# Optimization experiments

Measured on AMD Instinct MI355X. Metric: run time of the kernel, lower is better.

Reference implementation:

```python
import jax, jax.numpy as jnp
import numpy as np

BS, TS, NA, OS = 32, 256, 16, 512
HID, D, W = 1024, 128, 8            # sw_hidden_dim, sw_input_dim, sw_window_size
OUT, DEC, NACT = 512, 512, 30       # sw_output_dim, sw_decoder_hidden_layer, n_actions


def setup_inputs() -> dict:
    key = jax.random.key(0)
    ks = jax.random.split(key, 12)
    p = lambda k, shape: jax.random.normal(k, shape, jnp.float32) * 0.02
    return {
        "inputs": jax.random.normal(ks[0], (BS, TS, NA, OS), jnp.float32),
        "hidden_state": jnp.zeros((BS, NA, (W - 1) * D), jnp.float32),
        "w1": p(ks[1], (OS, HID)),        "b1": jnp.zeros((HID,), jnp.float32),
        "w2": p(ks[2], (HID, D)),         "b2": jnp.zeros((D,), jnp.float32),
        "w3": p(ks[3], (W * D, OUT)),     "b3": jnp.zeros((OUT,), jnp.float32),
        "w4": p(ks[4], (OUT, DEC)),       "b4": jnp.zeros((DEC,), jnp.float32),
        "w5": p(ks[5], (DEC, NACT)),      "b5": jnp.zeros((NACT,), jnp.float32),
    }


def reference(inputs, hidden_state, w1, b1, w2, b2, w3, b3, w4, b4, w5, b5):
    bs, ts, na, _ = inputs.shape
    # encoder: two pointwise MLP layers over (bs, ts, na, *)
    x = jax.nn.relu(inputs @ w1 + b1)          # (bs, ts, na, HID)
    x = jax.nn.relu(x @ w2 + b2)               # (bs, ts, na, D)
    # build the full frame sequence: W-1 hidden frames followed by ts encoded frames
    hid_frames = hidden_state.reshape(bs, na, W - 1, D)
    seq = jnp.concatenate([hid_frames, jnp.transpose(x, (0, 2, 1, 3))], axis=2)  # (bs, na, ts+W-1, D)
    # sliding windows: window at step t = frames [t, t+W) — vectorized over all t
    wins = jnp.stack([seq[:, :, i:i + ts, :] for i in range(W)], axis=3)  # (bs, na, ts, W, D)
    wins = wins.reshape(bs, na, ts, W * D)
    h = jax.nn.relu(wins @ w3 + b3)            # (bs, na, ts, OUT)
    h = jnp.transpose(h, (0, 2, 1, 3))         # (bs, ts, na, OUT)
    h = jax.nn.relu(h @ w4 + b4)               # (bs, ts, na, DEC)
    q = h @ w5 + b5                            # (bs, ts, na, NACT)
    # final carried window: last W-1 frames of the sequence, flattened per agent
    window = seq[:, :, ts:, :].reshape(bs, na, (W - 1) * D)
    return (q, window)
```

## Files before the change

### kernel.cpp

```cpp
#include <hip/hip_runtime.h>
#include <hip/hip_bf16.h>
#include <hip/hip_fp8.h>


#define DEVI __device__ __forceinline__

typedef float f32x4 __attribute__((ext_vector_type(4)));
typedef short s16x8 __attribute__((ext_vector_type(8)));
typedef short s16x4 __attribute__((ext_vector_type(4)));
typedef long long i64;

#define ROWS 131072
#define SEQ_T 263

#define W2P_OFF 524288
#define W3P_OFF 655360
#define W4P_OFF 1179648
#define W5P_OFF 1441792
#define WP_TOTAL 1458176

#define W3P8_BYTE_OFF 2916352
#define SEQ8_BYTE_OFF 3440640
#define BIG_BYTE_OFF 37388288

DEVI short f2bf(float f) {
  union { __hip_bfloat16 h; short s; } u;
  u.h = __float2bfloat16(f);
  return u.s;
}

DEVI unsigned int f2e4(float f) {
  union { __hip_fp8_e4m3 h; unsigned char c; } u;
  u.h = __hip_fp8_e4m3(f);
  return (unsigned int)u.c;
}

#if __has_builtin(__builtin_amdgcn_cvt_pk_fp8_f32)
DEVI unsigned int pk4e4(float a, float b, float c, float d) {
  int v = 0;
  v = __builtin_amdgcn_cvt_pk_fp8_f32(a, b, v, false);
  v = __builtin_amdgcn_cvt_pk_fp8_f32(c, d, v, true);
  return (unsigned int)v;
}
#else
DEVI unsigned int pk4e4(float a, float b, float c, float d) {
  return f2e4(a) | (f2e4(b) << 8) | (f2e4(c) << 16) | (f2e4(d) << 24);
}
#endif

DEVI f32x4 MFMA(s16x8 a, s16x8 b, f32x4 c) {
  return __builtin_amdgcn_mfma_f32_16x16x32_bf16(a, b, c, 0, 0, 0);
}
DEVI f32x4 MFMA8(i64 a, i64 b, f32x4 c) {
  return __builtin_amdgcn_mfma_f32_16x16x32_fp8_fp8(a, b, c, 0, 0, 0);
}

__global__ __launch_bounds__(256) void pack_w_kernel(
    const float* __restrict__ w1, const float* __restrict__ w2,
    const float* __restrict__ w3, const float* __restrict__ w4,
    const float* __restrict__ w5, short* __restrict__ wp)
{
  int idx = blockIdx.x * 256 + threadIdx.x;
  const float* src; int sh, Nsrc, local;
  if (idx < W2P_OFF)      { src = w1; sh = 4; Nsrc = 1024; local = idx; }
  else if (idx < W3P_OFF) { src = w2; sh = 5; Nsrc = 128;  local = idx - W2P_OFF; }
  else if (idx < W4P_OFF) { src = w3; sh = 5; Nsrc = 512;  local = idx - W3P_OFF; }
  else if (idx < W5P_OFF) { src = w4; sh = 4; Nsrc = 512;  local = idx - W4P_OFF; }
  else                    { src = w5; sh = 4; Nsrc = 30;   local = idx - W5P_OFF; }
  int j    = local & 7;
  int lane = (local >> 3) & 63;
  int rest = local >> 9;
  int k0   = rest & ((1 << sh) - 1);
  int n0   = rest >> sh;
  int k = (k0 << 5) + ((lane >> 4) << 3) + j;
  int n = (n0 << 4) + (lane & 15);
  float v = (n < Nsrc) ? src[k * Nsrc + n] : 0.f;
  wp[idx] = f2bf(v);
}

__global__ __launch_bounds__(256) void pack_w_fp8_kernel(
    const float* __restrict__ w1, const float* __restrict__ w2,
    const float* __restrict__ w3,
    unsigned char* __restrict__ wp8, unsigned char* __restrict__ w3p8)
{
  int t = blockIdx.x * 256 + threadIdx.x;
  const float* src; int nkshift, Nsrc, dt; unsigned char* dst;
  if (t < 65536)      { src = w1; dt = t;         nkshift = 4; Nsrc = 1024; dst = wp8; }
  else if (t < 81920) { src = w2; dt = t - 65536; nkshift = 5; Nsrc = 128;  dst = wp8 + 524288; }
  else                { src = w3; dt = t - 81920; nkshift = 5; Nsrc = 512;  dst = w3p8; }
  int lane = dt & 63;
  int rest = dt >> 6;
  int k0   = rest & ((1 << nkshift) - 1);
  int n0   = rest >> nkshift;
  int kb = (k0 << 5) + ((lane >> 4) << 3);
  int n  = (n0 << 4) + (lane & 15);
  float v[8];
  #pragma unroll
  for (int j = 0; j < 8; ++j) v[j] = src[(kb + j) * Nsrc + n];
  unsigned long long pk = (unsigned long long)pk4e4(v[0], v[1], v[2], v[3])
                        | ((unsigned long long)pk4e4(v[4], v[5], v[6], v[7]) << 32);
  *(unsigned long long*)(dst + (long)dt * 8) = pk;
}

__global__ __launch_bounds__(256) void hid_copy_kernel(
    const float* __restrict__ hid, unsigned char* __restrict__ seq8)
{
  int t = blockIdx.x * 256 + threadIdx.x;
  int j = t & 15;
  int r = t >> 4;
  int i = r % 7;
  int ba = r / 7;
  int s = j ^ i;
  const float* src = hid + (r << 7) + (j << 3);
  f32x4 a = *(const f32x4*)src;
  f32x4 b = *(const f32x4*)(src + 4);
  unsigned long long pk = (unsigned long long)pk4e4(a[0], a[1], a[2], a[3])
                        | ((unsigned long long)pk4e4(b[0], b[1], b[2], b[3]) << 32);
  *(unsigned long long*)(seq8 + (ba * SEQ_T + i) * 128 + s * 8) = pk;
}

__global__ __launch_bounds__(512, 4) void enc_kernel(
    const float* __restrict__ inp, const unsigned char* __restrict__ w1p8,
    const float* __restrict__ b1, const unsigned char* __restrict__ w2p8,
    const float* __restrict__ b2, unsigned char* __restrict__ seq8)
{
  __shared__ unsigned char As8[32768] __attribute__((aligned(16)));
  __shared__ unsigned char h1q8[32768] __attribute__((aligned(16)));
  const int tid = threadIdx.x;
  const int lane = tid & 63, wv = tid >> 6;
  const int l15 = lane & 15, lg = lane >> 4;
  const int rb = blockIdx.x << 6;

  #pragma unroll
  for (int it = 0; it < 8; ++it) {
    int g = it * 512 + tid;
    int row = g >> 6, j = g & 63;
    const float* s = inp + (long)(rb + row) * 512 + j * 8;
    f32x4 v0 = *(const f32x4*)s;
    f32x4 v1 = *(const f32x4*)(s + 4);
    unsigned long long pk = (unsigned long long)pk4e4(v0[0], v0[1], v0[2], v0[3])
                          | ((unsigned long long)pk4e4(v1[0], v1[1], v1[2], v1[3]) << 32);
    *(unsigned long long*)(As8 + (j << 9) + ((row ^ (j & 7)) << 3)) = pk;
  }
  __syncthreads();

  f32x4 z = {0.f, 0.f, 0.f, 0.f};
  f32x4 acc2[4] = {z, z, z, z};

  for (int p = 0; p < 2; ++p) {
    f32x4 acc1[4][4];
    #pragma unroll
    for (int i = 0; i < 4; ++i)
      #pragma unroll
      for (int j = 0; j < 4; ++j) acc1[i][j] = z;

    const unsigned char* wB = w1p8 + (((p * 32 + wv * 4) * 16) << 9) + lane * 8;

    i64 Wc[4];
    #pragma unroll
    for (int ci = 0; ci < 4; ++ci) Wc[ci] = *(const i64*)(wB + ((ci * 16) << 9));

    #pragma unroll 1
    for (int k0 = 0; k0 < 16; ++k0) {
      int kn = (k0 + 1) & 15;
      i64 Wn[4];
      #pragma unroll
      for (int ci = 0; ci < 4; ++ci) Wn[ci] = *(const i64*)(wB + ((ci * 16 + kn) << 9));
      int k2 = k0 * 4 + lg;
      int c = k2 & 7;
      i64 Xc[4];
      #pragma unroll
      for (int mi = 0; mi < 4; ++mi)
        Xc[mi] = *(const i64*)(As8 + (k2 << 9) + (((mi * 16 + l15) ^ c) << 3));
      #pragma unroll
      for (int ci = 0; ci < 4; ++ci)
        #pragma unroll
        for (int mi = 0; mi < 4; ++mi)
          acc1[ci][mi] = MFMA8(Wc[ci], Xc[mi], acc1[ci][mi]);
      #pragma unroll
      for (int ci = 0; ci < 4; ++ci) Wc[ci] = Wn[ci];
    }
    __syncthreads();
    #pragma unroll
    for (int ci = 0; ci < 4; ++ci) {
      f32x4 bv = *(const f32x4*)(b1 + p * 512 + wv * 64 + ci * 16 + lg * 4);
      int k2c = wv * 8 + ci * 2 + (lg >> 1);
      int half = (lg & 1) << 2;
      #pragma unroll
      for (int mi = 0; mi < 4; ++mi) {
        int m = mi * 16 + l15;
        unsigned int pk = pk4e4(fmaxf(acc1[ci][mi][0] + bv[0], 0.f),
                                fmaxf(acc1[ci][mi][1] + bv[1], 0.f),
                                fmaxf(acc1[ci][mi][2] + bv[2], 0.f),
                                fmaxf(acc1[ci][mi][3] + bv[3], 0.f));
        *(unsigned int*)(h1q8 + (k2c << 9) + (m << 3) + half) = pk;
      }
    }
    __syncthreads();
    const unsigned char* w2B = w2p8 + ((wv * 32 + p * 16) << 9) + lane * 8;
    i64 W2c = *(const i64*)(w2B);
    #pragma unroll 1
    for (int kk = 0; kk < 16; ++kk) {
      int kn = (kk + 1) & 15;
      i64 W2n = *(const i64*)(w2B + (kn << 9));
      i64 X2[4];
      #pragma unroll
      for (int mi = 0; mi < 4; ++mi)
        X2[mi] = *(const i64*)(h1q8 + ((kk * 4 + lg) << 9) + ((mi * 16 + l15) << 3));
      #pragma unroll
      for (int mi = 0; mi < 4; ++mi)
        acc2[mi] = MFMA8(W2c, X2[mi], acc2[mi]);
      W2c = W2n;
    }
  }
  __syncthreads();
  unsigned char* scr8 = As8;
  {
    f32x4 bv = *(const f32x4*)(b2 + wv * 16 + lg * 4);
    int gsb = wv * 2 + (lg >> 1);
    int off4 = (lg & 1) << 2;
    #pragma unroll
    for (int mi = 0; mi < 4; ++mi) {
      int m = mi * 16 + l15;
      int f7 = ((rb >> 4) + mi + 7) & 7;
      unsigned int pk = pk4e4(fmaxf(acc2[mi][0] + bv[0], 0.f),
                              fmaxf(acc2[mi][1] + bv[1], 0.f),
                              fmaxf(acc2[mi][2] + bv[2], 0.f),
                              fmaxf(acc2[mi][3] + bv[3], 0.f));
      int ls = (gsb ^ f7) ^ (m & 7);
      *(unsigned int*)(scr8 + m * 128 + ls * 8 + off4) = pk;
    }
  }
  __syncthreads();
  #pragma unroll
  for (int it = 0; it < 2; ++it) {
    int c = it * 512 + tid;
    int i = c >> 4, s = c & 15;
    unsigned long long v = *(const unsigned long long*)(scr8 + i * 128 + ((s ^ (i & 7)) << 3));
    int r = rb + i;
    int ba2 = ((r >> 12) << 4) + (r & 15);
    int t = (r >> 4) & 255;
    int f = t + 7;
    *(unsigned long long*)(seq8 + (ba2 * SEQ_T + f) * 128 + (s << 3)) = v;
  }
}

__global__ __launch_bounds__(256) void enc_hi_kernel(
    const float* __restrict__ inp, const short* __restrict__ w1p,
    const float* __restrict__ b1, const short* __restrict__ w2p,
    const float* __restrict__ b2, float* __restrict__ out)
{
  __shared__ short As[8192]  __attribute__((aligned(16)));
  __shared__ short h1s[16384] __attribute__((aligned(16)));
  const int tid = threadIdx.x;
  const int lane = tid & 63, wv = tid >> 6;
  const int l15 = lane & 15, lg = lane >> 4;
  const int b = blockIdx.x / 7, ti = blockIdx.x % 7;
  const int t = 249 + ti;
  const long row0 = (long)b * 4096 + t * 16;

  #pragma unroll
  for (int it = 0; it < 4; ++it) {
    int c = it * 256 + tid;
    int m = c >> 6, j = c & 63;
    const float* s = inp + (row0 + m) * 512 + j * 8;
    f32x4 v0 = *(const f32x4*)s;
    f32x4 v1 = *(const f32x4*)(s + 4);
    s16x8 o;
    o[0]=f2bf(v0[0]); o[1]=f2bf(v0[1]); o[2]=f2bf(v0[2]); o[3]=f2bf(v0[3]);
    o[4]=f2bf(v1[0]); o[5]=f2bf(v1[1]); o[6]=f2bf(v1[2]); o[7]=f2bf(v1[3]);
    *(s16x8*)((char*)As + (j << 8) + (((m ^ (j & 15)) & 15) << 4)) = o;
  }
  __syncthreads();

  f32x4 z = {0.f, 0.f, 0.f, 0.f};
  f32x4 acc1[16];
  #pragma unroll
  for (int i = 0; i < 16; ++i) acc1[i] = z;
  #pragma unroll 1
  for (int k0 = 0; k0 < 16; ++k0) {
    int k2 = k0 * 4 + lg;
    s16x8 X = *(const s16x8*)((const char*)As + (k2 << 8) + (((l15 ^ (k2 & 15)) & 15) << 4));
    #pragma unroll
    for (int ci = 0; ci < 16; ++ci) {
      s16x8 W = *(const s16x8*)(w1p + (((wv * 16 + ci) * 16 + k0) << 9) + lane * 8);
      acc1[ci] = MFMA(W, X, acc1[ci]);
    }
  }
  #pragma unroll
  for (int ci = 0; ci < 16; ++ci) {
    f32x4 bv = *(const f32x4*)(b1 + wv * 256 + ci * 16 + lg * 4);
    int k2c = wv * 32 + ci * 2 + (lg >> 1);
    int half = (lg & 1) << 3;
    s16x4 o;
    #pragma unroll
    for (int j = 0; j < 4; ++j)
      o[j] = f2bf(fmaxf(acc1[ci][j] + bv[j], 0.f));
    *(s16x4*)((char*)h1s + (k2c << 8) + (l15 << 4) + half) = o;
  }
  __syncthreads();
  f32x4 acc2[2] = {z, z};
  #pragma unroll 1
  for (int kk = 0; kk < 32; ++kk) {
    s16x8 X2 = *(const s16x8*)((const char*)h1s + ((kk * 4 + lg) << 8) + (l15 << 4));
    #pragma unroll
    for (int nf = 0; nf < 2; ++nf) {
      s16x8 W2 = *(const s16x8*)(w2p + (((wv * 2 + nf) * 32 + kk) << 9) + lane * 8);
      acc2[nf] = MFMA(W2, X2, acc2[nf]);
    }
  }
  #pragma unroll
  for (int nf = 0; nf < 2; ++nf) {
    #pragma unroll
    for (int rr = 0; rr < 4; ++rr) {
      int d = (wv * 2 + nf) * 16 + lg * 4 + rr;
      float v = fmaxf(acc2[nf][rr] + b2[d], 0.f);
      out[3932160 + (((b * 16 + l15) * 7 + ti) << 7) + d] = v;
    }
  }
}

__global__ __launch_bounds__(512, 4) void win_kernel(
    const unsigned char* __restrict__ seq8, const unsigned char* __restrict__ w3p8,
    const float* __restrict__ b3, short* __restrict__ h3p)
{
  __shared__ unsigned char sh8[17280] __attribute__((aligned(16)));
  __shared__ short rp[16384] __attribute__((aligned(16)));
  const int tid = threadIdx.x;
  const int lane = tid & 63, wid = tid >> 6;
  const int wm = wid >> 2, wn = wid & 3;
  const int l15 = lane & 15, lg = lane >> 4;
  const int bid = blockIdx.x;
  const int th = bid & 1, ba = bid >> 1;
  const int t0 = th << 7;

  const unsigned char* gsrc = seq8 + (ba * SEQ_T + t0) * 128;
  #pragma unroll
  for (int i = 0; i < 3; ++i) {
    int c = i * 512 + tid;
    if (c < 1080) *(s16x8*)&sh8[c * 16] = *(const s16x8*)(gsrc + c * 16);
  }
  __syncthreads();

  f32x4 z = {0.f, 0.f, 0.f, 0.f};
  for (int h = 0; h < 2; ++h) {
    f32x4 acc[4][4];
    #pragma unroll
    for (int i = 0; i < 4; ++i)
      #pragma unroll
      for (int j = 0; j < 4; ++j) acc[i][j] = z;

    const unsigned char* bB = w3p8 + (((h * 16 + wn * 4) * 32) << 9) + lane * 8;
    i64 bcur[4];
    #pragma unroll
    for (int nf = 0; nf < 4; ++nf) bcur[nf] = *(const i64*)(bB + ((nf * 32) << 9));

    #pragma unroll 1
    for (int kc = 0; kc < 32; ++kc) {
      int kn = (kc + 1) & 31;
      i64 bnxt[4];
      #pragma unroll
      for (int nf = 0; nf < 4; ++nf) bnxt[nf] = *(const i64*)(bB + ((nf * 32 + kn) << 9));
      int w = kc >> 2;
      int dslot = ((kc & 3) << 2) + lg;
      i64 av[4];
      #pragma unroll
      for (int mf = 0; mf < 4; ++mf) {
        int f = wm * 64 + mf * 16 + l15 + w;
        av[mf] = *(const i64*)(sh8 + f * 128 + ((dslot ^ (f & 7)) << 3));
      }
      #pragma unroll
      for (int nf = 0; nf < 4; ++nf)
        #pragma unroll
        for (int mf = 0; mf < 4; ++mf)
          acc[mf][nf] = MFMA8(av[mf], bcur[nf], acc[mf][nf]);
      #pragma unroll
      for (int nf = 0; nf < 4; ++nf) bcur[nf] = bnxt[nf];
    }

    for (int s = 0; s < 2; ++s) {
      __syncthreads();
      #pragma unroll
      for (int mf = 0; mf < 4; ++mf)
        #pragma unroll
        for (int e = 0; e < 2; ++e) {
          int nf = s * 2 + e;
          float bias = b3[h * 256 + wn * 64 + nf * 16 + l15];
          int lc = wn * 32 + e * 16 + l15;
          #pragma unroll
          for (int rr = 0; rr < 4; ++rr) {
            int row = wm * 64 + mf * 16 + lg * 4 + rr;
            float v = fmaxf(acc[mf][nf][rr] + bias, 0.f);
            int by = ((row << 8) + (lc << 1)) ^ ((row & 7) << 4);
            rp[by >> 1] = f2bf(v);
          }
        }
      __syncthreads();
      #pragma unroll
      for (int it = 0; it < 4; ++it) {
        int c = it * 512 + tid;
        int cl = c & 15, g = (c >> 4) & 3, kq = (c >> 6) & 3, tt = (c >> 8) & 7;
        int row = tt * 16 + cl;
        int by = ((row << 8) + (kq << 6) + (g << 4)) ^ ((row & 7) << 4);
        int k0g = h * 8 + kq * 2 + s;
        int mt = ba * 16 + th * 8 + tt;
        long dst = ((long)((mt * 16 + k0g) * 64 + g * 16 + cl)) << 3;
        *(s16x8*)(h3p + dst) = *(const s16x8*)((const char*)rp + by);
      }
    }
  }
}

__global__ __launch_bounds__(512, 4) void dec_kernel(
    const short* __restrict__ h3p, const short* __restrict__ w4p,
    const float* __restrict__ b4, const short* __restrict__ w5p,
    const float* __restrict__ b5, float* __restrict__ out)
{
  __shared__ short h4s[32768] __attribute__((aligned(16)));
  const int tid = threadIdx.x;
  const int lane = tid & 63, wid = tid >> 6;
  const int wm = wid >> 2, wn = wid & 3;
  const int mf5 = wid;
  const int l15 = lane & 15, lg = lane >> 4;
  const int rb = blockIdx.x << 7;

  f32x4 z = {0.f, 0.f, 0.f, 0.f};
  f32x4 acc5[2] = {z, z};
  const short* aBase = h3p + ((rb >> 4) + wm * 4) * 8192 + lane * 8;

  for (int h = 0; h < 2; ++h) {
    f32x4 acc[4][4];
    #pragma unroll
    for (int i = 0; i < 4; ++i)
      #pragma unroll
      for (int j = 0; j < 4; ++j) acc[i][j] = z;

    const short* bB = w4p + ((h * 16 + wn * 4) * 16) * 512 + lane * 8;
    s16x8 bcur[4];
    #pragma unroll
    for (int nf = 0; nf < 4; ++nf) bcur[nf] = *(const s16x8*)(bB + (nf * 16) * 512);

    #pragma unroll 1
    for (int k0 = 0; k0 < 16; ++k0) {
      int kn = (k0 + 1) & 15;
      s16x8 bnxt[4];
      #pragma unroll
      for (int nf = 0; nf < 4; ++nf) bnxt[nf] = *(const s16x8*)(bB + (nf * 16 + kn) * 512);
      s16x8 av[4];
      #pragma unroll
      for (int mf = 0; mf < 4; ++mf) av[mf] = *(const s16x8*)(aBase + mf * 8192 + k0 * 512);
      #pragma unroll
      for (int nf = 0; nf < 4; ++nf)
        #pragma unroll
        for (int mf = 0; mf < 4; ++mf)
          acc[mf][nf] = MFMA(av[mf], bcur[nf], acc[mf][nf]);
      #pragma unroll
      for (int nf = 0; nf < 4; ++nf) bcur[nf] = bnxt[nf];
    }
    __syncthreads();
    #pragma unroll
    for (int mf = 0; mf < 4; ++mf)
      #pragma unroll
      for (int nf = 0; nf < 4; ++nf) {
        int lc = wn * 64 + nf * 16 + l15;
        float bias = b4[h * 256 + lc];
        #pragma unroll
        for (int rr = 0; rr < 4; ++rr) {
          int row = wm * 64 + mf * 16 + lg * 4 + rr;
          float v = fmaxf(acc[mf][nf][rr] + bias, 0.f);
          int by = ((row << 9) + (lc << 1)) ^ ((row & 7) << 4);
          h4s[by >> 1] = f2bf(v);
        }
      }
    __syncthreads();
    #pragma unroll
    for (int kk = 0; kk < 8; ++kk) {
      int row = mf5 * 16 + l15;
      int by = ((row << 9) + (kk << 6) + (lg << 4)) ^ ((row & 7) << 4);
      s16x8 a0 = *(const s16x8*)((const char*)h4s + by);
      #pragma unroll
      for (int nf = 0; nf < 2; ++nf) {
        s16x8 wb = *(const s16x8*)(w5p + (nf * 16 + h * 8 + kk) * 512 + lane * 8);
        acc5[nf] = MFMA(a0, wb, acc5[nf]);
      }
    }
  }
  #pragma unroll
  for (int nf = 0; nf < 2; ++nf) {
    int col = nf * 16 + l15;
    if (col < 30) {
      float bias = b5[col];
      #pragma unroll
      for (int rr = 0; rr < 4; ++rr) {
        int row_ = rb + mf5 * 16 + lg * 4 + rr;
        int t = row_ & 255;
        int ba2 = row_ >> 8;
        int orow = (((ba2 >> 4) << 8) + t) * 16 + (ba2 & 15);
        out[orow * 30 + col] = acc5[nf][rr] + bias;
      }
    }
  }
}

extern "C" void kernel_launch(void* const* d_in, const int* in_sizes, int n_in,
                              void* d_out, int out_size, void* d_ws, size_t ws_size,
                              hipStream_t stream) {
  const float* inp = (const float*)d_in[0];
  const float* hid = (const float*)d_in[1];
  const float* w1  = (const float*)d_in[2];
  const float* b1  = (const float*)d_in[3];
  const float* w2  = (const float*)d_in[4];
  const float* b2  = (const float*)d_in[5];
  const float* w3  = (const float*)d_in[6];
  const float* b3  = (const float*)d_in[7];
  const float* w4  = (const float*)d_in[8];
  const float* b4  = (const float*)d_in[9];
  const float* w5  = (const float*)d_in[10];
  const float* b5  = (const float*)d_in[11];

  char* ws = (char*)d_ws;
  short* wp   = (short*)ws;
  short* w1p  = wp;
  short* w2p  = wp + W2P_OFF;
  short* w4p  = wp + W4P_OFF;
  short* w5p  = wp + W5P_OFF;
  unsigned char* w3p8 = (unsigned char*)(ws + W3P8_BYTE_OFF);
  unsigned char* seq8 = (unsigned char*)(ws + SEQ8_BYTE_OFF);
  short* h3p  = (short*)(ws + BIG_BYTE_OFF);
  unsigned char* w1p8 = (unsigned char*)h3p;
  unsigned char* w2p8 = w1p8 + 524288;
  float* out  = (float*)d_out;

  pack_w_kernel    <<<WP_TOTAL / 256, 256, 0, stream>>>(w1, w2, w3, w4, w5, wp);
  pack_w_fp8_kernel<<<576, 256, 0, stream>>>(w1, w2, w3, w1p8, w3p8);
  hid_copy_kernel  <<<224, 256, 0, stream>>>(hid, seq8);
  enc_kernel       <<<2048, 512, 0, stream>>>(inp, w1p8, b1, w2p8, b2, seq8);
  enc_hi_kernel    <<<224, 256, 0, stream>>>(inp, w1p, b1, w2p, b2, out);
  win_kernel       <<<1024, 512, 0, stream>>>(seq8, w3p8, b3, h3p);
  dec_kernel       <<<1024, 512, 0, stream>>>(h3p, w4p, b4, w5p, b5, out);
}
```

Before: 454.2 us.

## Use FP8 for decoder layer-4 GEMM and halve encoder h1 LDS buffer

The window kernel now writes its layer-3 activations as FP8 instead of bf16, and the decoder's first GEMM uses FP8 MFMA with a newly packed FP8 copy of w4. This halves the h3 intermediate traffic and doubles the MFMA rate for that GEMM. The encoder also splits the hidden layer into four passes instead of two, which halves the h1 shared buffer to raise occupancy. The cost is lower precision in the decoder input and weights, plus extra passes and barriers in the encoder.

New measurement: 471.1 us. 1.04x slower.

```diff
diff --git a/kernel.cpp b/kernel.cpp
--- a/kernel.cpp
+++ b/kernel.cpp
@@ -9,6 +9,7 @@
 typedef short s16x8 __attribute__((ext_vector_type(8)));
 typedef short s16x4 __attribute__((ext_vector_type(4)));
 typedef long long i64;
+typedef unsigned long long u64;
 
 #define ROWS 131072
 #define SEQ_T 263
@@ -21,12 +22,18 @@
 
 #define W3P8_BYTE_OFF 2916352
 #define SEQ8_BYTE_OFF 3440640
+#define W4P8_BYTE_OFF 20971520
 #define BIG_BYTE_OFF 37388288
 
 DEVI short f2bf(float f) {
   union { __hip_bfloat16 h; short s; } u;
   u.h = __float2bfloat16(f);
   return u.s;
+}
+DEVI float bf2f(short s) {
+  union { float f; unsigned int u; } v;
+  v.u = ((unsigned int)(unsigned short)s) << 16;
+  return v.f;
 }
 
 DEVI unsigned int f2e4(float f) {
@@ -80,14 +87,16 @@
 
 __global__ __launch_bounds__(256) void pack_w_fp8_kernel(
     const float* __restrict__ w1, const float* __restrict__ w2,
-    const float* __restrict__ w3,
-    unsigned char* __restrict__ wp8, unsigned char* __restrict__ w3p8)
+    const float* __restrict__ w3, const float* __restrict__ w4,
+    unsigned char* __restrict__ wp8, unsigned char* __restrict__ w3p8,
+    unsigned char* __restrict__ w4p8)
 {
   int t = blockIdx.x * 256 + threadIdx.x;
   const float* src; int nkshift, Nsrc, dt; unsigned char* dst;
-  if (t < 65536)      { src = w1; dt = t;         nkshift = 4; Nsrc = 1024; dst = wp8; }
-  else if (t < 81920) { src = w2; dt = t - 65536; nkshift = 5; Nsrc = 128;  dst = wp8 + 524288; }
-  else                { src = w3; dt = t - 81920; nkshift = 5; Nsrc = 512;  dst = w3p8; }
+  if (t < 65536)       { src = w1; dt = t;          nkshift = 4; Nsrc = 1024; dst = wp8; }
+  else if (t < 81920)  { src = w2; dt = t - 65536;  nkshift = 5; Nsrc = 128;  dst = wp8 + 524288; }
+  else if (t < 147456) { src = w3; dt = t - 81920;  nkshift = 5; Nsrc = 512;  dst = w3p8; }
+  else                 { src = w4; dt = t - 147456; nkshift = 4; Nsrc = 512;  dst = w4p8; }
   int lane = dt & 63;
   int rest = dt >> 6;
   int k0   = rest & ((1 << nkshift) - 1);
@@ -97,9 +106,9 @@
   float v[8];
   #pragma unroll
   for (int j = 0; j < 8; ++j) v[j] = src[(kb + j) * Nsrc + n];
-  unsigned long long pk = (unsigned long long)pk4e4(v[0], v[1], v[2], v[3])
-                        | ((unsigned long long)pk4e4(v[4], v[5], v[6], v[7]) << 32);
-  *(unsigned long long*)(dst + (long)dt * 8) = pk;
+  u64 pk = (u64)pk4e4(v[0], v[1], v[2], v[3])
+         | ((u64)pk4e4(v[4], v[5], v[6], v[7]) << 32);
+  *(u64*)(dst + (long)dt * 8) = pk;
 }
 
 __global__ __launch_bounds__(256) void hid_copy_kernel(
@@ -114,9 +123,9 @@
   const float* src = hid + (r << 7) + (j << 3);
   f32x4 a = *(const f32x4*)src;
   f32x4 b = *(const f32x4*)(src + 4);
-  unsigned long long pk = (unsigned long long)pk4e4(a[0], a[1], a[2], a[3])
-                        | ((unsigned long long)pk4e4(b[0], b[1], b[2], b[3]) << 32);
-  *(unsigned long long*)(seq8 + (ba * SEQ_T + i) * 128 + s * 8) = pk;
+  u64 pk = (u64)pk4e4(a[0], a[1], a[2], a[3])
+         | ((u64)pk4e4(b[0], b[1], b[2], b[3]) << 32);
+  *(u64*)(seq8 + (ba * SEQ_T + i) * 128 + s * 8) = pk;
 }
 
 __global__ __launch_bounds__(512, 4) void enc_kernel(
@@ -125,7 +134,7 @@
     const float* __restrict__ b2, unsigned char* __restrict__ seq8)
 {
   __shared__ unsigned char As8[32768] __attribute__((aligned(16)));
-  __shared__ unsigned char h1q8[32768] __attribute__((aligned(16)));
+  __shared__ unsigned char h1q8[16384] __attribute__((aligned(16)));
   const int tid = threadIdx.x;
   const int lane = tid & 63, wv = tid >> 6;
   const int l15 = lane & 15, lg = lane >> 4;
@@ -138,34 +147,33 @@
     const float* s = inp + (long)(rb + row) * 512 + j * 8;
     f32x4 v0 = *(const f32x4*)s;
     f32x4 v1 = *(const f32x4*)(s + 4);
-    unsigned long long pk = (unsigned long long)pk4e4(v0[0], v0[1], v0[2], v0[3])
-                          | ((unsigned long long)pk4e4(v1[0], v1[1], v1[2], v1[3]) << 32);
-    *(unsigned long long*)(As8 + (j << 9) + ((row ^ (j & 7)) << 3)) = pk;
+    u64 pk = (u64)pk4e4(v0[0], v0[1], v0[2], v0[3])
+           | ((u64)pk4e4(v1[0], v1[1], v1[2], v1[3]) << 32);
+    *(u64*)(As8 + (j << 9) + ((row ^ (j & 7)) << 3)) = pk;
   }
   __syncthreads();
 
   f32x4 z = {0.f, 0.f, 0.f, 0.f};
   f32x4 acc2[4] = {z, z, z, z};
 
-  for (int p = 0; p < 2; ++p) {
-    f32x4 acc1[4][4];
-    #pragma unroll
-    for (int i = 0; i < 4; ++i)
+  for (int p = 0; p < 4; ++p) {
+    f32x4 acc1[2][4];
+    #pragma unroll
+    for (int i = 0; i < 2; ++i)
       #pragma unroll
       for (int j = 0; j < 4; ++j) acc1[i][j] = z;
 
-    const unsigned char* wB = w1p8 + (((p * 32 + wv * 4) * 16) << 9) + lane * 8;
-
-    i64 Wc[4];
-    #pragma unroll
-    for (int ci = 0; ci < 4; ++ci) Wc[ci] = *(const i64*)(wB + ((ci * 16) << 9));
+    const unsigned char* wB = w1p8 + (((p * 16 + wv * 2) * 16) << 9) + lane * 8;
+
+    i64 Wc[2];
+    Wc[0] = *(const i64*)(wB);
+    Wc[1] = *(const i64*)(wB + (16 << 9));
 
     #pragma unroll 1
     for (int k0 = 0; k0 < 16; ++k0) {
       int kn = (k0 + 1) & 15;
-      i64 Wn[4];
-      #pragma unroll
-      for (int ci = 0; ci < 4; ++ci) Wn[ci] = *(const i64*)(wB + ((ci * 16 + kn) << 9));
+      i64 Wn0 = *(const i64*)(wB + (kn << 9));
+      i64 Wn1 = *(const i64*)(wB + ((16 + kn) << 9));
       int k2 = k0 * 4 + lg;
       int c = k2 & 7;
       i64 Xc[4];
@@ -173,18 +181,17 @@
       for (int mi = 0; mi < 4; ++mi)
         Xc[mi] = *(const i64*)(As8 + (k2 << 9) + (((mi * 16 + l15) ^ c) << 3));
       #pragma unroll
-      for (int ci = 0; ci < 4; ++ci)
-        #pragma unroll
-        for (int mi = 0; mi < 4; ++mi)
-          acc1[ci][mi] = MFMA8(Wc[ci], Xc[mi], acc1[ci][mi]);
-      #pragma unroll
-      for (int ci = 0; ci < 4; ++ci) Wc[ci] = Wn[ci];
+      for (int mi = 0; mi < 4; ++mi) {
+        acc1[0][mi] = MFMA8(Wc[0], Xc[mi], acc1[0][mi]);
+        acc1[1][mi] = MFMA8(Wc[1], Xc[mi], acc1[1][mi]);
+      }
+      Wc[0] = Wn0; Wc[1] = Wn1;
     }
     __syncthreads();
     #pragma unroll
-    for (int ci = 0; ci < 4; ++ci) {
-      f32x4 bv = *(const f32x4*)(b1 + p * 512 + wv * 64 + ci * 16 + lg * 4);
-      int k2c = wv * 8 + ci * 2 + (lg >> 1);
+    for (int ci = 0; ci < 2; ++ci) {
+      f32x4 bv = *(const f32x4*)(b1 + p * 256 + wv * 32 + ci * 16 + lg * 4);
+      int k2c = wv * 4 + ci * 2 + (lg >> 1);
       int half = (lg & 1) << 2;
       #pragma unroll
       for (int mi = 0; mi < 4; ++mi) {
@@ -197,11 +204,11 @@
       }
     }
     __syncthreads();
-    const unsigned char* w2B = w2p8 + ((wv * 32 + p * 16) << 9) + lane * 8;
+    const unsigned char* w2B = w2p8 + ((wv * 32 + p * 8) << 9) + lane * 8;
     i64 W2c = *(const i64*)(w2B);
     #pragma unroll 1
-    for (int kk = 0; kk < 16; ++kk) {
-      int kn = (kk + 1) & 15;
+    for (int kk = 0; kk < 8; ++kk) {
+      int kn = (kk + 1) & 7;
       i64 W2n = *(const i64*)(w2B + (kn << 9));
       i64 X2[4];
       #pragma unroll
@@ -236,12 +243,12 @@
   for (int it = 0; it < 2; ++it) {
     int c = it * 512 + tid;
     int i = c >> 4, s = c & 15;
-    unsigned long long v = *(const unsigned long long*)(scr8 + i * 128 + ((s ^ (i & 7)) << 3));
+    u64 v = *(const u64*)(scr8 + i * 128 + ((s ^ (i & 7)) << 3));
     int r = rb + i;
     int ba2 = ((r >> 12) << 4) + (r & 15);
     int t = (r >> 4) & 255;
     int f = t + 7;
-    *(unsigned long long*)(seq8 + (ba2 * SEQ_T + f) * 128 + (s << 3)) = v;
+    *(u64*)(seq8 + (ba2 * SEQ_T + f) * 128 + (s << 3)) = v;
   }
 }
 
@@ -322,7 +329,7 @@
 
 __global__ __launch_bounds__(512, 4) void win_kernel(
     const unsigned char* __restrict__ seq8, const unsigned char* __restrict__ w3p8,
-    const float* __restrict__ b3, short* __restrict__ h3p)
+    const float* __restrict__ b3, unsigned char* __restrict__ h3p8)
 {
   __shared__ unsigned char sh8[17280] __attribute__((aligned(16)));
   __shared__ short rp[16384] __attribute__((aligned(16)));
@@ -399,20 +406,24 @@
       #pragma unroll
       for (int it = 0; it < 4; ++it) {
         int c = it * 512 + tid;
-        int cl = c & 15, g = (c >> 4) & 3, kq = (c >> 6) & 3, tt = (c >> 8) & 7;
+        int cl = c & 15, g = (c >> 4) & 3, wni = (c >> 6) & 3, tt = (c >> 8) & 7;
         int row = tt * 16 + cl;
-        int by = ((row << 8) + (kq << 6) + (g << 4)) ^ ((row & 7) << 4);
-        int k0g = h * 8 + kq * 2 + s;
+        int lc = wni * 32 + g * 8;
+        int by = ((row << 8) + (lc << 1)) ^ ((row & 7) << 4);
+        s16x8 v = *(const s16x8*)((const char*)rp + by);
+        u64 pk = (u64)pk4e4(bf2f(v[0]), bf2f(v[1]), bf2f(v[2]), bf2f(v[3]))
+               | ((u64)pk4e4(bf2f(v[4]), bf2f(v[5]), bf2f(v[6]), bf2f(v[7])) << 32);
+        int k0g = h * 8 + wni * 2 + s;
         int mt = ba * 16 + th * 8 + tt;
         long dst = ((long)((mt * 16 + k0g) * 64 + g * 16 + cl)) << 3;
-        *(s16x8*)(h3p + dst) = *(const s16x8*)((const char*)rp + by);
+        *(u64*)(h3p8 + dst) = pk;
       }
     }
   }
 }
 
 __global__ __launch_bounds__(512, 4) void dec_kernel(
-    const short* __restrict__ h3p, const short* __restrict__ w4p,
+    const unsigned char* __restrict__ h3p8, const unsigned char* __restrict__ w4p8,
     const float* __restrict__ b4, const short* __restrict__ w5p,
     const float* __restrict__ b5, float* __restrict__ out)
 {
@@ -426,7 +437,7 @@
 
   f32x4 z = {0.f, 0.f, 0.f, 0.f};
   f32x4 acc5[2] = {z, z};
-  const short* aBase = h3p + ((rb >> 4) + wm * 4) * 8192 + lane * 8;
+  const unsigned char* aBase = h3p8 + (long)((rb >> 4) + wm * 4) * 8192 + lane * 8;
 
   for (int h = 0; h < 2; ++h) {
     f32x4 acc[4][4];
@@ -435,25 +446,25 @@
       #pragma unroll
       for (int j = 0; j < 4; ++j) acc[i][j] = z;
 
-    const short* bB = w4p + ((h * 16 + wn * 4) * 16) * 512 + lane * 8;
-    s16x8 bcur[4];
-    #pragma unroll
-    for (int nf = 0; nf < 4; ++nf) bcur[nf] = *(const s16x8*)(bB + (nf * 16) * 512);
+    const unsigned char* bB = w4p8 + (((h * 16 + wn * 4) * 16) << 9) + lane * 8;
+    i64 bcur[4];
+    #pragma unroll
+    for (int nf = 0; nf < 4; ++nf) bcur[nf] = *(const i64*)(bB + ((nf * 16) << 9));
 
     #pragma unroll 1
     for (int k0 = 0; k0 < 16; ++k0) {
       int kn = (k0 + 1) & 15;
-      s16x8 bnxt[4];
-      #pragma unroll
-      for (int nf = 0; nf < 4; ++nf) bnxt[nf] = *(const s16x8*)(bB + (nf * 16 + kn) * 512);
-      s16x8 av[4];
-      #pragma unroll
-      for (int mf = 0; mf < 4; ++mf) av[mf] = *(const s16x8*)(aBase + mf * 8192 + k0 * 512);
+      i64 bnxt[4];
+      #pragma unroll
+      for (int nf = 0; nf < 4; ++nf) bnxt[nf] = *(const i64*)(bB + ((nf * 16 + kn) << 9));
+      i64 av[4];
+      #pragma unroll
+      for (int mf = 0; mf < 4; ++mf) av[mf] = *(const i64*)(aBase + mf * 8192 + k0 * 512);
       #pragma unroll
       for (int nf = 0; nf < 4; ++nf)
         #pragma unroll
         for (int mf = 0; mf < 4; ++mf)
-          acc[mf][nf] = MFMA(av[mf], bcur[nf], acc[mf][nf]);
+          acc[mf][nf] = MFMA8(av[mf], bcur[nf], acc[mf][nf]);
       #pragma unroll
       for (int nf = 0; nf < 4; ++nf) bcur[nf] = bnxt[nf];
     }
@@ -522,20 +533,20 @@
   short* wp   = (short*)ws;
   short* w1p  = wp;
   short* w2p  = wp + W2P_OFF;
-  short* w4p  = wp + W4P_OFF;
   short* w5p  = wp + W5P_OFF;
   unsigned char* w3p8 = (unsigned char*)(ws + W3P8_BYTE_OFF);
   unsigned char* seq8 = (unsigned char*)(ws + SEQ8_BYTE_OFF);
-  short* h3p  = (short*)(ws + BIG_BYTE_OFF);
-  unsigned char* w1p8 = (unsigned char*)h3p;
+  unsigned char* w4p8 = (unsigned char*)(ws + W4P8_BYTE_OFF);
+  unsigned char* h3p8 = (unsigned char*)(ws + BIG_BYTE_OFF);
+  unsigned char* w1p8 = h3p8;
   unsigned char* w2p8 = w1p8 + 524288;
   float* out  = (float*)d_out;
 
   pack_w_kernel    <<<WP_TOTAL / 256, 256, 0, stream>>>(w1, w2, w3, w4, w5, wp);
-  pack_w_fp8_kernel<<<576, 256, 0, stream>>>(w1, w2, w3, w1p8, w3p8);
+  pack_w_fp8_kernel<<<704, 256, 0, stream>>>(w1, w2, w3, w4, w1p8, w3p8, w4p8);
   hid_copy_kernel  <<<224, 256, 0, stream>>>(hid, seq8);
   enc_kernel       <<<2048, 512, 0, stream>>>(inp, w1p8, b1, w2p8, b2, seq8);
   enc_hi_kernel    <<<224, 256, 0, stream>>>(inp, w1p, b1, w2p, b2, out);
-  win_kernel       <<<1024, 512, 0, stream>>>(seq8, w3p8, b3, h3p);
-  dec_kernel       <<<1024, 512, 0, stream>>>(h3p, w4p, b4, w5p, b5, out);
-}
+  win_kernel       <<<1024, 512, 0, stream>>>(seq8, w3p8, b3, h3p8);
+  dec_kernel       <<<1024, 512, 0, stream>>>(h3p8, w4p8, b4, w5p, b5, out);
+}
```
